# Optimization experiments

Hardware: AMD Instinct MI355X
Metric: run time of the kernel (lower is better)

The kernel has to match this reference:

```python
import jax, jax.numpy as jnp
import numpy as np

N_USER, N_MOVIE = 100000, 20000
D_USER, D_MOVIE = 32, 64
H = 64
E = 2000000
B = 200000


def _sage(x_src, x_dst, src, dst, W_l, b_l, W_r, n_dst):
    # PyG SAGEConv: out = lin_l(mean_{j in N(i)} x_j) + lin_r(x_i)
    msg = x_src[src]                                   # [E, d_src] gather
    agg = jax.ops.segment_sum(msg, dst, num_segments=n_dst)
    cnt = jax.ops.segment_sum(jnp.ones((src.shape[0],), x_src.dtype), dst,
                              num_segments=n_dst)
    mean = agg / jnp.maximum(cnt, 1.0)[:, None]        # [n_dst, d_src]
    return mean @ W_l + b_l + x_dst @ W_r


def setup_inputs() -> dict:
    key = jax.random.key(0)
    ks = jax.random.split(key, 24)
    f = jnp.float32

    def lin(k, din, dout):
        s = 1.0 / np.sqrt(din)
        return jax.random.uniform(k, (din, dout), f, -s, s)

    inp = {
        'x_user': jax.random.normal(ks[0], (N_USER, D_USER), f),
        'x_movie': jax.random.normal(ks[1], (N_MOVIE, D_MOVIE), f),
        'src_um': jax.random.randint(ks[2], (E,), 0, N_USER),
        'dst_um': jax.random.randint(ks[3], (E,), 0, N_MOVIE),
        'src_mu': jax.random.randint(ks[4], (E,), 0, N_MOVIE),
        'dst_mu': jax.random.randint(ks[5], (E,), 0, N_USER),
        'label_row': jax.random.randint(ks[6], (B,), 0, N_USER),
        'label_col': jax.random.randint(ks[7], (B,), 0, N_MOVIE),
        # layer 1, edge type user->movie (dst=movie): lin_l on aggregated src (user feats)
        'W1_um_l': lin(ks[8], D_USER, H), 'b1_um': jnp.zeros((H,), f),
        'W1_um_r': lin(ks[9], D_MOVIE, H),
        # layer 1, edge type movie->user (dst=user)
        'W1_mu_l': lin(ks[10], D_MOVIE, H), 'b1_mu': jnp.zeros((H,), f),
        'W1_mu_r': lin(ks[11], D_USER, H),
        # layer 2 (inputs are hidden H for both types)
        'W2_um_l': lin(ks[12], H, H), 'b2_um': jnp.zeros((H,), f),
        'W2_um_r': lin(ks[13], H, H),
        'W2_mu_l': lin(ks[14], H, H), 'b2_mu': jnp.zeros((H,), f),
        'W2_mu_r': lin(ks[15], H, H),
        # head: Linear(2H, 2)
        'W_lin': lin(ks[16], 2 * H, 2), 'b_lin': jnp.zeros((2,), f),
    }
    return inp


def reference(x_user, x_movie, src_um, dst_um, src_mu, dst_mu,
              label_row, label_col,
              W1_um_l, b1_um, W1_um_r, W1_mu_l, b1_mu, W1_mu_r,
              W2_um_l, b2_um, W2_um_r, W2_mu_l, b2_mu, W2_mu_r,
              W_lin, b_lin):
    # layer 1 (to_hetero aggr='sum': each node type has one incoming edge type)
    h_movie = _sage(x_user, x_movie, src_um, dst_um, W1_um_l, b1_um, W1_um_r, N_MOVIE)
    h_user = _sage(x_movie, x_user, src_mu, dst_mu, W1_mu_l, b1_mu, W1_mu_r, N_USER)
    h_movie = jax.nn.relu(h_movie)
    h_user = jax.nn.relu(h_user)
    # layer 2
    z_movie = _sage(h_user, h_movie, src_um, dst_um, W2_um_l, b2_um, W2_um_r, N_MOVIE)
    z_user = _sage(h_movie, h_user, src_mu, dst_mu, W2_mu_l, b2_mu, W2_mu_r, N_USER)
    # head
    concat = jnp.concatenate([z_user[label_row], z_movie[label_col]], axis=-1)
    out = concat @ W_lin + b_lin                       # [B, 2]
    mu = out[:, 0]
    sigma = jax.nn.softplus(out[:, 1]) + 1e-6
    return mu, sigma
```

## Files before the change

kernel.cpp:

```cpp
#include <hip/hip_runtime.h>
#include <hip/hip_bf16.h>
#include <hip/hip_fp16.h>
#include <type_traits>

#define NB_UM 79
#define NB_MU 98
#define NBALL 177
#define NBLK 256

using f16x8 = __attribute__((ext_vector_type(8))) _Float16;
using f32x4 = __attribute__((ext_vector_type(4))) float;


__global__ __launch_bounds__(256) void cast_half2(const float* __restrict__ a,
                                                  __half* __restrict__ ah, int na,
                                                  const float* __restrict__ b,
                                                  __half* __restrict__ bh, int nb) {
    int i = blockIdx.x * blockDim.x + threadIdx.x;
    int st = gridDim.x * blockDim.x;
    for (int k = i; k < na / 2; k += st) {
        float2 v = ((const float2*)a)[k];
        ((__half2*)ah)[k] = __floats2half2_rn(v.x, v.y);
    }
    for (int k = i; k < nb / 2; k += st) {
        float2 v = ((const float2*)b)[k];
        ((__half2*)bh)[k] = __floats2half2_rn(v.x, v.y);
    }
}


__global__ __launch_bounds__(1024) void hist_part(const int* __restrict__ dst_um,
                                                  const int* __restrict__ dst_mu,
                                                  int* __restrict__ histM, int E, int chunk) {
    __shared__ int h[NBALL];
    for (int i = threadIdx.x; i < NBALL; i += 1024) h[i] = 0;
    __syncthreads();
    int blk = blockIdx.x;
    int s = blk * chunk, e = min(E, s + chunk);
    if (s < e) {
        int n4 = (e - s) >> 2;
        const int4* du4 = (const int4*)(dst_um + s);
        const int4* dm4 = (const int4*)(dst_mu + s);
        for (int i = threadIdx.x; i < n4; i += 1024) {
            int4 d = du4[i];
            atomicAdd(&h[d.x >> 8], 1);
            atomicAdd(&h[d.y >> 8], 1);
            atomicAdd(&h[d.z >> 8], 1);
            atomicAdd(&h[d.w >> 8], 1);
            int4 m = dm4[i];
            atomicAdd(&h[NB_UM + (m.x >> 10)], 1);
            atomicAdd(&h[NB_UM + (m.y >> 10)], 1);
            atomicAdd(&h[NB_UM + (m.z >> 10)], 1);
            atomicAdd(&h[NB_UM + (m.w >> 10)], 1);
        }
        for (int i = s + (n4 << 2) + threadIdx.x; i < e; i += 1024) {
            atomicAdd(&h[dst_um[i] >> 8], 1);
            atomicAdd(&h[NB_UM + (dst_mu[i] >> 10)], 1);
        }
    }
    __syncthreads();
    for (int i = threadIdx.x; i < NBALL; i += 1024) histM[i * NBLK + blk] = h[i];
}


__global__ __launch_bounds__(256) void bucket_totals(int* __restrict__ histM,
                                                     int* __restrict__ btot, int nball) {
    int w = (blockIdx.x * blockDim.x + threadIdx.x) >> 6;
    int lane = threadIdx.x & 63;
    if (w >= nball) return;
    int* row = histM + w * NBLK;
    int v[4];
    int s = 0;
#pragma unroll
    for (int i = 0; i < 4; i++) {
        int c = row[lane * 4 + i];
        v[i] = s;
        s += c;
    }
    int incl = s;
    for (int d = 1; d < 64; d <<= 1) {
        int y = __shfl_up(incl, d, 64);
        if (lane >= d) incl += y;
    }
    int excl = incl - s;
#pragma unroll
    for (int i = 0; i < 4; i++) row[lane * 4 + i] = excl + v[i];
    if (lane == 63) btot[w] = incl;
}


__global__ __launch_bounds__(256) void boff_scan(const int* __restrict__ btot,
                                                 int* __restrict__ boff, int nball,
                                                 int* __restrict__ off_um, int NM,
                                                 int* __restrict__ off_mu, int NU, int E) {
    __shared__ int sdata[256];
    int t = threadIdx.x;
    int v[8];
    int sum = 0;
#pragma unroll
    for (int i = 0; i < 8; i++) {
        int idx = t * 8 + i;
        int c = (idx < nball) ? btot[idx] : 0;
        v[i] = sum;
        sum += c;
    }
    sdata[t] = sum;
    __syncthreads();
    for (int s = 1; s < 256; s <<= 1) {
        int y = (t >= s) ? sdata[t - s] : 0;
        __syncthreads();
        sdata[t] += y;
        __syncthreads();
    }
    int base = (t == 0) ? 0 : sdata[t - 1];
#pragma unroll
    for (int i = 0; i < 8; i++) {
        int idx = t * 8 + i;
        if (idx < nball) boff[idx] = base + v[i];
    }
    if (t == 0) {
        boff[nball] = 2 * E;
        off_um[NM] = E;
        off_mu[NU] = E;
    }
}


__global__ __launch_bounds__(1024) void partition2(const int* __restrict__ src_um,
                                                   const int* __restrict__ dst_um,
                                                   const int* __restrict__ src_mu,
                                                   const int* __restrict__ dst_mu,
                                                   const int* __restrict__ histM,
                                                   const int* __restrict__ boff,
                                                   int* __restrict__ tmp, int E, int chunk) {
    __shared__ int cur[NBALL];
    int blk = blockIdx.x;
    for (int i = threadIdx.x; i < NBALL; i += 1024)
        cur[i] = histM[i * NBLK + blk] + boff[i];
    __syncthreads();
    int s = blk * chunk, e = min(E, s + chunk);
    if (s >= e) return;
    int n4 = (e - s) >> 2;
    const int4* su4 = (const int4*)(src_um + s);
    const int4* du4 = (const int4*)(dst_um + s);
    const int4* sm4 = (const int4*)(src_mu + s);
    const int4* dm4 = (const int4*)(dst_mu + s);
    for (int i = threadIdx.x; i < n4; i += 1024) {
        int4 sv = su4[i];
        int4 dv = du4[i];
        int p;
        p = atomicAdd(&cur[dv.x >> 8], 1); tmp[p] = sv.x | ((dv.x & 255) << 20);
        p = atomicAdd(&cur[dv.y >> 8], 1); tmp[p] = sv.y | ((dv.y & 255) << 20);
        p = atomicAdd(&cur[dv.z >> 8], 1); tmp[p] = sv.z | ((dv.z & 255) << 20);
        p = atomicAdd(&cur[dv.w >> 8], 1); tmp[p] = sv.w | ((dv.w & 255) << 20);
        int4 sv2 = sm4[i];
        int4 dv2 = dm4[i];
        p = atomicAdd(&cur[NB_UM + (dv2.x >> 10)], 1); tmp[p] = sv2.x | ((dv2.x & 1023) << 20);
        p = atomicAdd(&cur[NB_UM + (dv2.y >> 10)], 1); tmp[p] = sv2.y | ((dv2.y & 1023) << 20);
        p = atomicAdd(&cur[NB_UM + (dv2.z >> 10)], 1); tmp[p] = sv2.z | ((dv2.z & 1023) << 20);
        p = atomicAdd(&cur[NB_UM + (dv2.w >> 10)], 1); tmp[p] = sv2.w | ((dv2.w & 1023) << 20);
    }
    for (int i = s + (n4 << 2) + threadIdx.x; i < e; i += 1024) {
        int d = dst_um[i];
        int p = atomicAdd(&cur[d >> 8], 1);
        tmp[p] = src_um[i] | ((d & 255) << 20);
        int d2 = dst_mu[i];
        int q = atomicAdd(&cur[NB_UM + (d2 >> 10)], 1);
        tmp[q] = src_mu[i] | ((d2 & 1023) << 20);
    }
}


__global__ __launch_bounds__(1024) void scatter_both(const int* __restrict__ tmp,
                                                     const int* __restrict__ boff,
                                                     int* __restrict__ off_um,
                                                     int* __restrict__ csr_um, int NM,
                                                     int* __restrict__ off_mu,
                                                     int* __restrict__ csr_mu, int NU, int E) {
    __shared__ int lcnt[1024];
    __shared__ int lcur[1024];
    __shared__ int sdata[1024];
    int b = blockIdx.x;
    int um = (b < NB_UM);
    int W = um ? 256 : 1024;
    int n = um ? NM : NU;
    int sub = um ? 0 : E;
    int* off = um ? off_um : off_mu;
    int* csr = um ? csr_um : csr_mu;
    int rowbase = (um ? b : (b - NB_UM)) * W;
    int t = threadIdx.x;
    int s = boff[b], e = boff[b + 1];
    for (int j = t; j < W; j += 1024) lcnt[j] = 0;
    __syncthreads();
    for (int i = s + t; i < e; i += 1024) atomicAdd(&lcnt[tmp[i] >> 20], 1);
    __syncthreads();
    int myc = (t < W) ? lcnt[t] : 0;
    sdata[t] = myc;
    __syncthreads();
    for (int d = 1; d < 1024; d <<= 1) {
        int y = (t >= d) ? sdata[t - d] : 0;
        __syncthreads();
        sdata[t] += y;
        __syncthreads();
    }
    if (t < W) lcur[t] = s + sdata[t] - myc;
    __syncthreads();
    for (int j = t; j < W; j += 1024)
        if (rowbase + j < n) off[rowbase + j] = lcur[j] - sub;
    __syncthreads();
    for (int i = s + t; i < e; i += 1024) {
        int vv = tmp[i];
        int p = atomicAdd(&lcur[vv >> 20], 1);
        csr[p - sub] = vv & 0xFFFFF;
    }
}


__device__ __forceinline__ void acc8(float* a, uint4 r) {
    const __half2* h = reinterpret_cast<const __half2*>(&r);
#pragma unroll
    for (int j = 0; j < 4; j++) {
        float2 f = __half22float2(h[j]);
        a[2 * j] += f.x;
        a[2 * j + 1] += f.y;
    }
}

template <int D>
__device__ __forceinline__ void agg_body(const int* __restrict__ csr,
                                         const int* __restrict__ off,
                                         const __half* __restrict__ xh,
                                         float* __restrict__ out, int nrows,
                                         int bid, int nblocks) {
    constexpr int L = D / 8;
    int gid = (bid * 256 + (int)threadIdx.x) / L;
    int lg = threadIdx.x & (L - 1);
    int ngroups = (nblocks * 256) / L;
    int c8 = lg * 8;
    for (int row = gid; row < nrows; row += ngroups) {
        int s = off[row], e = off[row + 1];
        float a[8] = {0.f, 0.f, 0.f, 0.f, 0.f, 0.f, 0.f, 0.f};
        int k = s;
        for (; k + 4 <= e; k += 4) {
            int i0 = csr[k], i1 = csr[k + 1], i2 = csr[k + 2], i3 = csr[k + 3];
            uint4 r0 = *(const uint4*)&xh[(long)i0 * D + c8];
            uint4 r1 = *(const uint4*)&xh[(long)i1 * D + c8];
            uint4 r2 = *(const uint4*)&xh[(long)i2 * D + c8];
            uint4 r3 = *(const uint4*)&xh[(long)i3 * D + c8];
            acc8(a, r0); acc8(a, r1); acc8(a, r2); acc8(a, r3);
        }
        for (; k < e; ++k) {
            uint4 r0 = *(const uint4*)&xh[(long)csr[k] * D + c8];
            acc8(a, r0);
        }
        float inv = 1.0f / fmaxf((float)(e - s), 1.0f);
        float4 q0 = make_float4(a[0] * inv, a[1] * inv, a[2] * inv, a[3] * inv);
        float4 q1 = make_float4(a[4] * inv, a[5] * inv, a[6] * inv, a[7] * inv);
        *(float4*)&out[(long)row * D + c8] = q0;
        *(float4*)&out[(long)row * D + c8 + 4] = q1;
    }
}

__global__ __launch_bounds__(256) void agg_dual_l1(const int* __restrict__ csr_um,
                                                   const int* __restrict__ off_um,
                                                   const __half* __restrict__ xh_u,
                                                   float* __restrict__ A_m, int NM, int g1,
                                                   const int* __restrict__ csr_mu,
                                                   const int* __restrict__ off_mu,
                                                   const __half* __restrict__ xh_m,
                                                   float* __restrict__ A_u, int NU) {
    if ((int)blockIdx.x < g1)
        agg_body<32>(csr_um, off_um, xh_u, A_m, NM, blockIdx.x, g1);
    else
        agg_body<64>(csr_mu, off_mu, xh_m, A_u, NU, blockIdx.x - g1, gridDim.x - g1);
}

__global__ __launch_bounds__(256) void agg_dual_l2(const int* __restrict__ csr_um,
                                                   const int* __restrict__ off_um,
                                                   const __half* __restrict__ Hh_u,
                                                   float* __restrict__ A_m, int NM, int g1,
                                                   const int* __restrict__ csr_mu,
                                                   const int* __restrict__ off_mu,
                                                   const __half* __restrict__ Hh_m,
                                                   float* __restrict__ A_u, int NU) {
    if ((int)blockIdx.x < g1)
        agg_body<64>(csr_um, off_um, Hh_u, A_m, NM, blockIdx.x, g1);
    else
        agg_body<64>(csr_mu, off_mu, Hh_m, A_u, NU, blockIdx.x - g1, gridDim.x - g1);
}


template <int Dm, int Dd, bool RELU, typename TX, typename TO>
__device__ __forceinline__ void dense_body(char* smemraw,
                                           const float* __restrict__ mean,
                                           const TX* __restrict__ xd,
                                           const float* __restrict__ Wl,
                                           const float* __restrict__ Wr,
                                           const float* __restrict__ bias,
                                           TO* __restrict__ out, int n, int bid) {
    constexpr int K = Dm + Dd;
    constexpr int SAP = K + 8;
    _Float16* sA = (_Float16*)smemraw;
    _Float16* sWt = sA + 64 * SAP;
    float* sb = (float*)(sWt + 64 * SAP);
    int t = threadIdx.x;
    int R0 = bid * 64;

    for (int i = t; i < K * 16; i += 256) {
        int k = i >> 4, c = (i & 15) * 4;
        float4 v = (k < Dm) ? *(const float4*)&Wl[k * 64 + c]
                            : *(const float4*)&Wr[(k - Dm) * 64 + c];
        sWt[(c + 0) * SAP + k] = (_Float16)v.x;
        sWt[(c + 1) * SAP + k] = (_Float16)v.y;
        sWt[(c + 2) * SAP + k] = (_Float16)v.z;
        sWt[(c + 3) * SAP + k] = (_Float16)v.w;
    }
    if (t < 64) sb[t] = bias[t];
    constexpr int QR = K / 4;
    for (int i = t; i < 64 * QR; i += 256) {
        int r = i / QR, c = (i % QR) * 4;
        int gr = R0 + r;
        float4 v = make_float4(0.f, 0.f, 0.f, 0.f);
        if (gr < n) {
            if (c < Dm) {
                v = *(const float4*)&mean[(long)gr * Dm + c];
            } else {
                if constexpr (std::is_same<TX, __half>::value) {
                    const __half* p = &xd[(long)gr * Dd + (c - Dm)];
                    v = make_float4(__half2float(p[0]), __half2float(p[1]),
                                    __half2float(p[2]), __half2float(p[3]));
                } else {
                    v = *(const float4*)&xd[(long)gr * Dd + (c - Dm)];
                }
            }
        }
        _Float16* p = &sA[r * SAP + c];
        p[0] = (_Float16)v.x; p[1] = (_Float16)v.y;
        p[2] = (_Float16)v.z; p[3] = (_Float16)v.w;
    }
    __syncthreads();

    int w = t >> 6, lane = t & 63;
    int lr = lane & 15, lg = lane >> 4;
    f32x4 acc[4];
#pragma unroll
    for (int nt = 0; nt < 4; nt++) {
        float bb = sb[16 * nt + lr];
        acc[nt][0] = bb; acc[nt][1] = bb; acc[nt][2] = bb; acc[nt][3] = bb;
    }
    int arow = 16 * w + lr;
#pragma unroll
    for (int kk = 0; kk < K / 32; kk++) {
        int k0 = kk * 32 + 8 * lg;
        f16x8 a = *(const f16x8*)&sA[arow * SAP + k0];
#pragma unroll
        for (int nt = 0; nt < 4; nt++) {
            f16x8 b = *(const f16x8*)&sWt[(16 * nt + lr) * SAP + k0];
            acc[nt] = __builtin_amdgcn_mfma_f32_16x16x32_f16(a, b, acc[nt], 0, 0, 0);
        }
    }
#pragma unroll
    for (int nt = 0; nt < 4; nt++) {
#pragma unroll
        for (int r = 0; r < 4; r++) {
            int gr = R0 + 16 * w + lg * 4 + r;
            if (gr >= n) continue;
            float vv = acc[nt][r];
            if (RELU) vv = fmaxf(vv, 0.f);
            int gc = 16 * nt + lr;
            if constexpr (std::is_same<TO, __half>::value) {
                out[(long)gr * 64 + gc] = __float2half(vv);
            } else {
                out[(long)gr * 64 + gc] = vv;
            }
        }
    }
}

#define DENSE_SMEM_BYTES (64 * 136 * 2 * 2 + 256)

__global__ __launch_bounds__(256) void dense_dual_l1(const float* __restrict__ A_m,
                                                     const float* __restrict__ x_movie,
                                                     const float* __restrict__ W1l_um,
                                                     const float* __restrict__ W1r_um,
                                                     const float* __restrict__ b1_um,
                                                     __half* __restrict__ Hh_m, int NM, int g1,
                                                     const float* __restrict__ A_u,
                                                     const float* __restrict__ x_user,
                                                     const float* __restrict__ W1l_mu,
                                                     const float* __restrict__ W1r_mu,
                                                     const float* __restrict__ b1_mu,
                                                     __half* __restrict__ Hh_u, int NU) {
    __shared__ __align__(16) char smem[DENSE_SMEM_BYTES];
    if ((int)blockIdx.x < g1)
        dense_body<32, 64, true, float, __half>(smem, A_m, x_movie, W1l_um, W1r_um, b1_um,
                                                Hh_m, NM, blockIdx.x);
    else
        dense_body<64, 32, true, float, __half>(smem, A_u, x_user, W1l_mu, W1r_mu, b1_mu,
                                                Hh_u, NU, blockIdx.x - g1);
}

__global__ __launch_bounds__(256) void dense_dual_l2(float* __restrict__ A_m,
                                                     const __half* __restrict__ Hh_m,
                                                     const float* __restrict__ W2l_um,
                                                     const float* __restrict__ W2r_um,
                                                     const float* __restrict__ b2_um,
                                                     int NM, int g1,
                                                     float* __restrict__ A_u,
                                                     const __half* __restrict__ Hh_u,
                                                     const float* __restrict__ W2l_mu,
                                                     const float* __restrict__ W2r_mu,
                                                     const float* __restrict__ b2_mu,
                                                     int NU) {
    __shared__ __align__(16) char smem[DENSE_SMEM_BYTES];
    if ((int)blockIdx.x < g1)
        dense_body<64, 64, false, __half, float>(smem, A_m, Hh_m, W2l_um, W2r_um, b2_um,
                                                 A_m, NM, blockIdx.x);
    else
        dense_body<64, 64, false, __half, float>(smem, A_u, Hh_u, W2l_mu, W2r_mu, b2_mu,
                                                 A_u, NU, blockIdx.x - g1);
}


__global__ __launch_bounds__(256) void proj_dual(const float* __restrict__ zu,
                                                 const float* __restrict__ zm,
                                                 const float* __restrict__ Wlin,
                                                 const float* __restrict__ blin,
                                                 float2* __restrict__ pu,
                                                 float2* __restrict__ pm,
                                                 int NU, int NM, int gu) {
    int isu = ((int)blockIdx.x < gu);
    const float* z = isu ? zu : zm;
    float2* p = isu ? pu : pm;
    int n = isu ? NU : NM;
    int woff = isu ? 0 : 64;
    int bid = isu ? blockIdx.x : blockIdx.x - gu;
    __shared__ float sW0[64], sW1[64];
    int t = threadIdx.x;
    if (t < 64) {
        sW0[t] = Wlin[(woff + t) * 2 + 0];
        sW1[t] = Wlin[(woff + t) * 2 + 1];
    }
    __syncthreads();
    float b0 = isu ? blin[0] : 0.f;
    float b1 = isu ? blin[1] : 0.f;
    int lane = t & 63;
    int w = t >> 6;
    int lr = lane & 15, q = lane >> 4;
    int row = bid * 16 + w * 4 + q;
    if (row >= n) return;
    float4 zv = *(const float4*)&z[(long)row * 64 + lr * 4];
    float p0 = zv.x * sW0[lr * 4] + zv.y * sW0[lr * 4 + 1] + zv.z * sW0[lr * 4 + 2] + zv.w * sW0[lr * 4 + 3];
    float p1 = zv.x * sW1[lr * 4] + zv.y * sW1[lr * 4 + 1] + zv.z * sW1[lr * 4 + 2] + zv.w * sW1[lr * 4 + 3];
#pragma unroll
    for (int m = 1; m < 16; m <<= 1) {
        p0 += __shfl_xor(p0, m, 64);
        p1 += __shfl_xor(p1, m, 64);
    }
    if (lr == 0) p[row] = make_float2(p0 + b0, p1 + b1);
}


__global__ __launch_bounds__(256) void head_gather(const float2* __restrict__ pu,
                                                   const float2* __restrict__ pm,
                                                   const int* __restrict__ lrow,
                                                   const int* __restrict__ lcol,
                                                   float* __restrict__ out, int B) {
    int i = blockIdx.x * blockDim.x + threadIdx.x;
    int st = gridDim.x * blockDim.x;
    for (int b = i; b < B; b += st) {
        float2 a = pu[lrow[b]];
        float2 d = pm[lcol[b]];
        float m = a.x + d.x;
        float x = a.y + d.y;
        float sp = fmaxf(x, 0.f) + log1pf(expf(-fabsf(x)));
        out[b] = m;
        out[B + b] = sp + 1e-6f;
    }
}


extern "C" void kernel_launch(void* const* d_in, const int* in_sizes, int n_in,
                              void* d_out, int out_size, void* d_ws, size_t ws_size,
                              hipStream_t stream) {
    const float* x_user  = (const float*)d_in[0];
    const float* x_movie = (const float*)d_in[1];
    const int* src_um = (const int*)d_in[2];
    const int* dst_um = (const int*)d_in[3];
    const int* src_mu = (const int*)d_in[4];
    const int* dst_mu = (const int*)d_in[5];
    const int* lrow = (const int*)d_in[6];
    const int* lcol = (const int*)d_in[7];
    const float* W1_um_l = (const float*)d_in[8];
    const float* b1_um   = (const float*)d_in[9];
    const float* W1_um_r = (const float*)d_in[10];
    const float* W1_mu_l = (const float*)d_in[11];
    const float* b1_mu   = (const float*)d_in[12];
    const float* W1_mu_r = (const float*)d_in[13];
    const float* W2_um_l = (const float*)d_in[14];
    const float* b2_um   = (const float*)d_in[15];
    const float* W2_um_r = (const float*)d_in[16];
    const float* W2_mu_l = (const float*)d_in[17];
    const float* b2_mu   = (const float*)d_in[18];
    const float* W2_mu_r = (const float*)d_in[19];
    const float* W_lin   = (const float*)d_in[20];
    const float* b_lin   = (const float*)d_in[21];
    float* out = (float*)d_out;

    const int E  = in_sizes[2];
    const int B  = in_sizes[6];
    const int NU = in_sizes[0] / 32;
    const int NM = in_sizes[1] / 64;

    char* wsp = (char*)d_ws;
    size_t o = 0;
    auto alloc = [&](size_t bytes) {
        size_t p = o;
        o += (bytes + 255) & ~(size_t)255;
        return (void*)(wsp + p);
    };
    int* off_um = (int*)alloc((size_t)(NM + 1) * 4);
    int* off_mu = (int*)alloc((size_t)(NU + 1) * 4);
    int* btot   = (int*)alloc((NBALL) * 4);
    int* boff   = (int*)alloc((NBALL + 1) * 4);
    int* csr_um = (int*)alloc((size_t)E * 4);
    int* csr_mu = (int*)alloc((size_t)E * 4);
    float* A_m  = (float*)alloc((size_t)NM * 64 * 4);
    float* A_u  = (float*)alloc((size_t)NU * 64 * 4);
    __half* Hh_m = (__half*)alloc((size_t)NM * 64 * 2);
    __half* Hh_u = (__half*)alloc((size_t)NU * 64 * 2);
    __half* xh_u = (__half*)alloc((size_t)NU * 32 * 2);
    __half* xh_m = (__half*)alloc((size_t)NM * 64 * 2);
    float2* pu  = (float2*)alloc((size_t)NU * 8);
    float2* pm  = (float2*)alloc((size_t)NM * 8);
    (void)ws_size;

    int* tmp   = (int*)A_u;
    int* histM = (int*)A_m;

    const int chunk = (((E + NBLK - 1) / NBLK) + 3) & ~3;

    cast_half2<<<512, 256, 0, stream>>>(x_user, xh_u, NU * 32, x_movie, xh_m, NM * 64);

    hist_part<<<NBLK, 1024, 0, stream>>>(dst_um, dst_mu, histM, E, chunk);
    bucket_totals<<<(NBALL + 3) / 4, 256, 0, stream>>>(histM, btot, NBALL);
    boff_scan<<<1, 256, 0, stream>>>(btot, boff, NBALL, off_um, NM, off_mu, NU, E);
    partition2<<<NBLK, 1024, 0, stream>>>(src_um, dst_um, src_mu, dst_mu, histM, boff,
                                          tmp, E, chunk);
    scatter_both<<<NBALL, 1024, 0, stream>>>(tmp, boff, off_um, csr_um, NM,
                                             off_mu, csr_mu, NU, E);

    {
        int g1 = (NM * 4 + 255) / 256;
        int g2 = (NU * 8 + 255) / 256;
        agg_dual_l1<<<g1 + g2, 256, 0, stream>>>(csr_um, off_um, xh_u, A_m, NM, g1,
                                                 csr_mu, off_mu, xh_m, A_u, NU);
        int d1 = (NM + 63) / 64, d2 = (NU + 63) / 64;
        dense_dual_l1<<<d1 + d2, 256, 0, stream>>>(A_m, x_movie, W1_um_l, W1_um_r, b1_um,
                                                   Hh_m, NM, d1,
                                                   A_u, x_user, W1_mu_l, W1_mu_r, b1_mu,
                                                   Hh_u, NU);
    }

    {
        int g1 = (NM * 8 + 255) / 256;
        int g2 = (NU * 8 + 255) / 256;
        agg_dual_l2<<<g1 + g2, 256, 0, stream>>>(csr_um, off_um, Hh_u, A_m, NM, g1,
                                                 csr_mu, off_mu, Hh_m, A_u, NU);
        int d1 = (NM + 63) / 64, d2 = (NU + 63) / 64;
        dense_dual_l2<<<d1 + d2, 256, 0, stream>>>(A_m, Hh_m, W2_um_l, W2_um_r, b2_um, NM, d1,
                                                   A_u, Hh_u, W2_mu_l, W2_mu_r, b2_mu, NU);
    }

    {
        int gu = (NU + 15) / 16, gm = (NM + 15) / 16;
        proj_dual<<<gu + gm, 256, 0, stream>>>(A_u, A_m, W_lin, b_lin, pu, pm, NU, NM, gu);
    }
    head_gather<<<1024, 256, 0, stream>>>(pu, pm, lrow, lcol, out, B);
}
```

Before: 245.8 us.

## Store aggregated means and layer-2 outputs in fp16, fuse cast/hist and scan kernels

Aggregation outputs and the layer-2 dense outputs are now written as fp16 instead of fp32, halving their write and read traffic and letting the dense kernel copy them straight into shared memory. The input cast kernel is merged into the histogram kernel as extra blocks, and the bucket-totals and offset-scan kernels are merged into a single one-block kernel, cutting launch count. The tmp partition buffer gets its own allocation because A_u no longer has room for it in fp16. Precision of intermediate means and of z is reduced to fp16, and the merged scan now runs in one block.

New measurement: 247.8 us. Within noise of the previous version (+0.8%).

```diff
diff --git a/kernel.cpp b/kernel.cpp
--- a/kernel.cpp
+++ b/kernel.cpp
@@ -7,31 +7,32 @@
 #define NB_MU 98
 #define NBALL 177
 #define NBLK 256
+#define CAST_BLKS 64
 
 using f16x8 = __attribute__((ext_vector_type(8))) _Float16;
 using f32x4 = __attribute__((ext_vector_type(4))) float;
 
 
-__global__ __launch_bounds__(256) void cast_half2(const float* __restrict__ a,
-                                                  __half* __restrict__ ah, int na,
-                                                  const float* __restrict__ b,
-                                                  __half* __restrict__ bh, int nb) {
-    int i = blockIdx.x * blockDim.x + threadIdx.x;
-    int st = gridDim.x * blockDim.x;
-    for (int k = i; k < na / 2; k += st) {
-        float2 v = ((const float2*)a)[k];
-        ((__half2*)ah)[k] = __floats2half2_rn(v.x, v.y);
-    }
-    for (int k = i; k < nb / 2; k += st) {
-        float2 v = ((const float2*)b)[k];
-        ((__half2*)bh)[k] = __floats2half2_rn(v.x, v.y);
-    }
-}
-
-
-__global__ __launch_bounds__(1024) void hist_part(const int* __restrict__ dst_um,
+__global__ __launch_bounds__(1024) void hist_cast(const int* __restrict__ dst_um,
                                                   const int* __restrict__ dst_mu,
-                                                  int* __restrict__ histM, int E, int chunk) {
+                                                  int* __restrict__ histM, int E, int chunk,
+                                                  const float* __restrict__ xu,
+                                                  __half* __restrict__ xhu, int nu,
+                                                  const float* __restrict__ xm,
+                                                  __half* __restrict__ xhm, int nm) {
+    if ((int)blockIdx.x >= NBLK) {
+        int i = ((int)blockIdx.x - NBLK) * 1024 + threadIdx.x;
+        int st = CAST_BLKS * 1024;
+        for (int k = i; k < nu / 2; k += st) {
+            float2 v = ((const float2*)xu)[k];
+            ((__half2*)xhu)[k] = __floats2half2_rn(v.x, v.y);
+        }
+        for (int k = i; k < nm / 2; k += st) {
+            float2 v = ((const float2*)xm)[k];
+            ((__half2*)xhm)[k] = __floats2half2_rn(v.x, v.y);
+        }
+        return;
+    }
     __shared__ int h[NBALL];
     for (int i = threadIdx.x; i < NBALL; i += 1024) h[i] = 0;
     __syncthreads();
@@ -63,63 +64,51 @@
 }
 
 
-__global__ __launch_bounds__(256) void bucket_totals(int* __restrict__ histM,
-                                                     int* __restrict__ btot, int nball) {
-    int w = (blockIdx.x * blockDim.x + threadIdx.x) >> 6;
-    int lane = threadIdx.x & 63;
-    if (w >= nball) return;
-    int* row = histM + w * NBLK;
-    int v[4];
-    int s = 0;
-#pragma unroll
-    for (int i = 0; i < 4; i++) {
-        int c = row[lane * 4 + i];
-        v[i] = s;
-        s += c;
-    }
-    int incl = s;
-    for (int d = 1; d < 64; d <<= 1) {
-        int y = __shfl_up(incl, d, 64);
-        if (lane >= d) incl += y;
-    }
-    int excl = incl - s;
-#pragma unroll
-    for (int i = 0; i < 4; i++) row[lane * 4 + i] = excl + v[i];
-    if (lane == 63) btot[w] = incl;
-}
-
-
-__global__ __launch_bounds__(256) void boff_scan(const int* __restrict__ btot,
-                                                 int* __restrict__ boff, int nball,
-                                                 int* __restrict__ off_um, int NM,
-                                                 int* __restrict__ off_mu, int NU, int E) {
+__global__ __launch_bounds__(1024) void totals_scan(int* __restrict__ histM,
+                                                    int* __restrict__ boff,
+                                                    int* __restrict__ off_um, int NM,
+                                                    int* __restrict__ off_mu, int NU, int E) {
+    __shared__ int sbt[NBALL];
     __shared__ int sdata[256];
     int t = threadIdx.x;
-    int v[8];
-    int sum = 0;
-#pragma unroll
-    for (int i = 0; i < 8; i++) {
-        int idx = t * 8 + i;
-        int c = (idx < nball) ? btot[idx] : 0;
-        v[i] = sum;
-        sum += c;
-    }
-    sdata[t] = sum;
-    __syncthreads();
-    for (int s = 1; s < 256; s <<= 1) {
-        int y = (t >= s) ? sdata[t - s] : 0;
+    int wid = t >> 6, lane = t & 63;
+    for (int w = wid; w < NBALL; w += 16) {
+        int* row = histM + w * NBLK;
+        int v[4];
+        int s = 0;
+#pragma unroll
+        for (int i = 0; i < 4; i++) {
+            int c = row[lane * 4 + i];
+            v[i] = s;
+            s += c;
+        }
+        int incl = s;
+        for (int d = 1; d < 64; d <<= 1) {
+            int y = __shfl_up(incl, d, 64);
+            if (lane >= d) incl += y;
+        }
+        int excl = incl - s;
+#pragma unroll
+        for (int i = 0; i < 4; i++) row[lane * 4 + i] = excl + v[i];
+        if (lane == 63) sbt[w] = incl;
+    }
+    __syncthreads();
+    int v0 = 0;
+    if (t < 256) {
+        v0 = (t < NBALL) ? sbt[t] : 0;
+        sdata[t] = v0;
+    }
+    __syncthreads();
+    for (int d = 1; d < 256; d <<= 1) {
+        int y = 0;
+        if (t < 256 && t >= d) y = sdata[t - d];
         __syncthreads();
-        sdata[t] += y;
+        if (t < 256) sdata[t] += y;
         __syncthreads();
     }
-    int base = (t == 0) ? 0 : sdata[t - 1];
-#pragma unroll
-    for (int i = 0; i < 8; i++) {
-        int idx = t * 8 + i;
-        if (idx < nball) boff[idx] = base + v[i];
-    }
+    if (t < NBALL) boff[t] = sdata[t] - v0;
     if (t == 0) {
-        boff[nball] = 2 * E;
+        boff[NBALL] = 2 * E;
         off_um[NM] = E;
         off_mu[NU] = E;
     }
@@ -230,7 +219,7 @@
 __device__ __forceinline__ void agg_body(const int* __restrict__ csr,
                                          const int* __restrict__ off,
                                          const __half* __restrict__ xh,
-                                         float* __restrict__ out, int nrows,
+                                         __half* __restrict__ out, int nrows,
                                          int bid, int nblocks) {
     constexpr int L = D / 8;
     int gid = (bid * 256 + (int)threadIdx.x) / L;
@@ -254,21 +243,25 @@
             acc8(a, r0);
         }
         float inv = 1.0f / fmaxf((float)(e - s), 1.0f);
-        float4 q0 = make_float4(a[0] * inv, a[1] * inv, a[2] * inv, a[3] * inv);
-        float4 q1 = make_float4(a[4] * inv, a[5] * inv, a[6] * inv, a[7] * inv);
-        *(float4*)&out[(long)row * D + c8] = q0;
-        *(float4*)&out[(long)row * D + c8 + 4] = q1;
+        __half2 h0 = __floats2half2_rn(a[0] * inv, a[1] * inv);
+        __half2 h1 = __floats2half2_rn(a[2] * inv, a[3] * inv);
+        __half2 h2 = __floats2half2_rn(a[4] * inv, a[5] * inv);
+        __half2 h3 = __floats2half2_rn(a[6] * inv, a[7] * inv);
+        uint4 w;
+        w.x = *(unsigned*)&h0; w.y = *(unsigned*)&h1;
+        w.z = *(unsigned*)&h2; w.w = *(unsigned*)&h3;
+        *(uint4*)&out[(long)row * D + c8] = w;
     }
 }
 
 __global__ __launch_bounds__(256) void agg_dual_l1(const int* __restrict__ csr_um,
                                                    const int* __restrict__ off_um,
                                                    const __half* __restrict__ xh_u,
-                                                   float* __restrict__ A_m, int NM, int g1,
+                                                   __half* __restrict__ A_m, int NM, int g1,
                                                    const int* __restrict__ csr_mu,
                                                    const int* __restrict__ off_mu,
                                                    const __half* __restrict__ xh_m,
-                                                   float* __restrict__ A_u, int NU) {
+                                                   __half* __restrict__ A_u, int NU) {
     if ((int)blockIdx.x < g1)
         agg_body<32>(csr_um, off_um, xh_u, A_m, NM, blockIdx.x, g1);
     else
@@ -278,11 +271,11 @@
 __global__ __launch_bounds__(256) void agg_dual_l2(const int* __restrict__ csr_um,
                                                    const int* __restrict__ off_um,
                                                    const __half* __restrict__ Hh_u,
-                                                   float* __restrict__ A_m, int NM, int g1,
+                                                   __half* __restrict__ A_m, int NM, int g1,
                                                    const int* __restrict__ csr_mu,
                                                    const int* __restrict__ off_mu,
                                                    const __half* __restrict__ Hh_m,
-                                                   float* __restrict__ A_u, int NU) {
+                                                   __half* __restrict__ A_u, int NU) {
     if ((int)blockIdx.x < g1)
         agg_body<64>(csr_um, off_um, Hh_u, A_m, NM, blockIdx.x, g1);
     else
@@ -290,14 +283,14 @@
 }
 
 
-template <int Dm, int Dd, bool RELU, typename TX, typename TO>
+template <int Dm, int Dd, bool RELU, typename TX>
 __device__ __forceinline__ void dense_body(char* smemraw,
-                                           const float* __restrict__ mean,
+                                           const __half* __restrict__ mean,
                                            const TX* __restrict__ xd,
                                            const float* __restrict__ Wl,
                                            const float* __restrict__ Wr,
                                            const float* __restrict__ bias,
-                                           TO* __restrict__ out, int n, int bid) {
+                                           __half* __restrict__ out, int n, int bid) {
     constexpr int K = Dm + Dd;
     constexpr int SAP = K + 8;
     _Float16* sA = (_Float16*)smemraw;
@@ -320,23 +313,23 @@
     for (int i = t; i < 64 * QR; i += 256) {
         int r = i / QR, c = (i % QR) * 4;
         int gr = R0 + r;
-        float4 v = make_float4(0.f, 0.f, 0.f, 0.f);
+        _Float16* p = &sA[r * SAP + c];
         if (gr < n) {
             if (c < Dm) {
-                v = *(const float4*)&mean[(long)gr * Dm + c];
+                *(uint2*)p = *(const uint2*)&mean[(long)gr * Dm + c];
             } else {
                 if constexpr (std::is_same<TX, __half>::value) {
-                    const __half* p = &xd[(long)gr * Dd + (c - Dm)];
-                    v = make_float4(__half2float(p[0]), __half2float(p[1]),
-                                    __half2float(p[2]), __half2float(p[3]));
+                    *(uint2*)p = *(const uint2*)&xd[(long)gr * Dd + (c - Dm)];
                 } else {
-                    v = *(const float4*)&xd[(long)gr * Dd + (c - Dm)];
+                    float4 v = *(const float4*)&xd[(long)gr * Dd + (c - Dm)];
+                    p[0] = (_Float16)v.x; p[1] = (_Float16)v.y;
+                    p[2] = (_Float16)v.z; p[3] = (_Float16)v.w;
                 }
             }
-        }
-        _Float16* p = &sA[r * SAP + c];
-        p[0] = (_Float16)v.x; p[1] = (_Float16)v.y;
-        p[2] = (_Float16)v.z; p[3] = (_Float16)v.w;
+        } else {
+            p[0] = (_Float16)0.f; p[1] = (_Float16)0.f;
+            p[2] = (_Float16)0.f; p[3] = (_Float16)0.f;
+        }
     }
     __syncthreads();
 
@@ -367,25 +360,20 @@
             if (gr >= n) continue;
             float vv = acc[nt][r];
             if (RELU) vv = fmaxf(vv, 0.f);
-            int gc = 16 * nt + lr;
-            if constexpr (std::is_same<TO, __half>::value) {
-                out[(long)gr * 64 + gc] = __float2half(vv);
-            } else {
-                out[(long)gr * 64 + gc] = vv;
-            }
+            out[(long)gr * 64 + 16 * nt + lr] = __float2half(vv);
         }
     }
 }
 
 #define DENSE_SMEM_BYTES (64 * 136 * 2 * 2 + 256)
 
-__global__ __launch_bounds__(256) void dense_dual_l1(const float* __restrict__ A_m,
+__global__ __launch_bounds__(256) void dense_dual_l1(const __half* __restrict__ A_m,
                                                      const float* __restrict__ x_movie,
                                                      const float* __restrict__ W1l_um,
                                                      const float* __restrict__ W1r_um,
                                                      const float* __restrict__ b1_um,
                                                      __half* __restrict__ Hh_m, int NM, int g1,
-                                                     const float* __restrict__ A_u,
+                                                     const __half* __restrict__ A_u,
                                                      const float* __restrict__ x_user,
                                                      const float* __restrict__ W1l_mu,
                                                      const float* __restrict__ W1r_mu,
@@ -393,20 +381,20 @@
                                                      __half* __restrict__ Hh_u, int NU) {
     __shared__ __align__(16) char smem[DENSE_SMEM_BYTES];
     if ((int)blockIdx.x < g1)
-        dense_body<32, 64, true, float, __half>(smem, A_m, x_movie, W1l_um, W1r_um, b1_um,
-                                                Hh_m, NM, blockIdx.x);
+        dense_body<32, 64, true, float>(smem, A_m, x_movie, W1l_um, W1r_um, b1_um,
+                                        Hh_m, NM, blockIdx.x);
     else
-        dense_body<64, 32, true, float, __half>(smem, A_u, x_user, W1l_mu, W1r_mu, b1_mu,
-                                                Hh_u, NU, blockIdx.x - g1);
-}
-
-__global__ __launch_bounds__(256) void dense_dual_l2(float* __restrict__ A_m,
+        dense_body<64, 32, true, float>(smem, A_u, x_user, W1l_mu, W1r_mu, b1_mu,
+                                        Hh_u, NU, blockIdx.x - g1);
+}
+
+__global__ __launch_bounds__(256) void dense_dual_l2(__half* __restrict__ A_m,
                                                      const __half* __restrict__ Hh_m,
                                                      const float* __restrict__ W2l_um,
                                                      const float* __restrict__ W2r_um,
                                                      const float* __restrict__ b2_um,
                                                      int NM, int g1,
-                                                     float* __restrict__ A_u,
+                                                     __half* __restrict__ A_u,
                                                      const __half* __restrict__ Hh_u,
                                                      const float* __restrict__ W2l_mu,
                                                      const float* __restrict__ W2r_mu,
@@ -414,23 +402,23 @@
                                                      int NU) {
     __shared__ __align__(16) char smem[DENSE_SMEM_BYTES];
     if ((int)blockIdx.x < g1)
-        dense_body<64, 64, false, __half, float>(smem, A_m, Hh_m, W2l_um, W2r_um, b2_um,
-                                                 A_m, NM, blockIdx.x);
+        dense_body<64, 64, false, __half>(smem, A_m, Hh_m, W2l_um, W2r_um, b2_um,
+                                          A_m, NM, blockIdx.x);
     else
-        dense_body<64, 64, false, __half, float>(smem, A_u, Hh_u, W2l_mu, W2r_mu, b2_mu,
-                                                 A_u, NU, blockIdx.x - g1);
-}
-
-
-__global__ __launch_bounds__(256) void proj_dual(const float* __restrict__ zu,
-                                                 const float* __restrict__ zm,
+        dense_body<64, 64, false, __half>(smem, A_u, Hh_u, W2l_mu, W2r_mu, b2_mu,
+                                          A_u, NU, blockIdx.x - g1);
+}
+
+
+__global__ __launch_bounds__(256) void proj_dual(const __half* __restrict__ zu,
+                                                 const __half* __restrict__ zm,
                                                  const float* __restrict__ Wlin,
                                                  const float* __restrict__ blin,
                                                  float2* __restrict__ pu,
                                                  float2* __restrict__ pm,
                                                  int NU, int NM, int gu) {
     int isu = ((int)blockIdx.x < gu);
-    const float* z = isu ? zu : zm;
+    const __half* z = isu ? zu : zm;
     float2* p = isu ? pu : pm;
     int n = isu ? NU : NM;
     int woff = isu ? 0 : 64;
@@ -449,9 +437,13 @@
     int lr = lane & 15, q = lane >> 4;
     int row = bid * 16 + w * 4 + q;
     if (row >= n) return;
-    float4 zv = *(const float4*)&z[(long)row * 64 + lr * 4];
-    float p0 = zv.x * sW0[lr * 4] + zv.y * sW0[lr * 4 + 1] + zv.z * sW0[lr * 4 + 2] + zv.w * sW0[lr * 4 + 3];
-    float p1 = zv.x * sW1[lr * 4] + zv.y * sW1[lr * 4 + 1] + zv.z * sW1[lr * 4 + 2] + zv.w * sW1[lr * 4 + 3];
+    uint2 raw = *(const uint2*)&z[(long)row * 64 + lr * 4];
+    __half2 z01 = *(__half2*)&raw.x;
+    __half2 z23 = *(__half2*)&raw.y;
+    float2 f01 = __half22float2(z01);
+    float2 f23 = __half22float2(z23);
+    float p0 = f01.x * sW0[lr * 4] + f01.y * sW0[lr * 4 + 1] + f23.x * sW0[lr * 4 + 2] + f23.y * sW0[lr * 4 + 3];
+    float p1 = f01.x * sW1[lr * 4] + f01.y * sW1[lr * 4 + 1] + f23.x * sW1[lr * 4 + 2] + f23.y * sW1[lr * 4 + 3];
 #pragma unroll
     for (int m = 1; m < 16; m <<= 1) {
         p0 += __shfl_xor(p0, m, 64);
@@ -521,12 +513,12 @@
     };
     int* off_um = (int*)alloc((size_t)(NM + 1) * 4);
     int* off_mu = (int*)alloc((size_t)(NU + 1) * 4);
-    int* btot   = (int*)alloc((NBALL) * 4);
     int* boff   = (int*)alloc((NBALL + 1) * 4);
     int* csr_um = (int*)alloc((size_t)E * 4);
     int* csr_mu = (int*)alloc((size_t)E * 4);
-    float* A_m  = (float*)alloc((size_t)NM * 64 * 4);
-    float* A_u  = (float*)alloc((size_t)NU * 64 * 4);
+    int* tmp    = (int*)alloc((size_t)2 * E * 4);
+    __half* A_m  = (__half*)alloc((size_t)NM * 64 * 2);
+    __half* A_u  = (__half*)alloc((size_t)NU * 64 * 2);
     __half* Hh_m = (__half*)alloc((size_t)NM * 64 * 2);
     __half* Hh_u = (__half*)alloc((size_t)NU * 64 * 2);
     __half* xh_u = (__half*)alloc((size_t)NU * 32 * 2);
@@ -535,16 +527,14 @@
     float2* pm  = (float2*)alloc((size_t)NM * 8);
     (void)ws_size;
 
-    int* tmp   = (int*)A_u;
     int* histM = (int*)A_m;
 
     const int chunk = (((E + NBLK - 1) / NBLK) + 3) & ~3;
 
-    cast_half2<<<512, 256, 0, stream>>>(x_user, xh_u, NU * 32, x_movie, xh_m, NM * 64);
-
-    hist_part<<<NBLK, 1024, 0, stream>>>(dst_um, dst_mu, histM, E, chunk);
-    bucket_totals<<<(NBALL + 3) / 4, 256, 0, stream>>>(histM, btot, NBALL);
-    boff_scan<<<1, 256, 0, stream>>>(btot, boff, NBALL, off_um, NM, off_mu, NU, E);
+    hist_cast<<<NBLK + CAST_BLKS, 1024, 0, stream>>>(dst_um, dst_mu, histM, E, chunk,
+                                                     x_user, xh_u, NU * 32,
+                                                     x_movie, xh_m, NM * 64);
+    totals_scan<<<1, 1024, 0, stream>>>(histM, boff, off_um, NM, off_mu, NU, E);
     partition2<<<NBLK, 1024, 0, stream>>>(src_um, dst_um, src_mu, dst_mu, histM, boff,
                                           tmp, E, chunk);
     scatter_both<<<NBALL, 1024, 0, stream>>>(tmp, boff, off_um, csr_um, NM,
```
